# Kernel optimization log

Measured on AMD Instinct MI355X. Metric: run time of the kernel, lower is better.

Reference implementation:

```python
import math
import jax, jax.numpy as jnp
import numpy as np

HIDDEN = 1024
HEADS = 16
HEAD_DIM = HIDDEN // HEADS
PRIME = 7
MAX_ITERS = 10
ENT_THRESH = 0.2
PRIME_SCALE = 1.0 / math.sqrt(PRIME * HEAD_DIM)
EPS = 1e-6


def setup_inputs() -> dict:
    key = jax.random.key(0)
    ks = jax.random.split(key, 6)
    B, S = 2, 2048
    w = 0.02
    return {
        "hidden_states": jax.random.normal(ks[0], (B, S, HIDDEN), jnp.float32),
        "q_w": jax.random.normal(ks[1], (HIDDEN, HIDDEN), jnp.float32) * w,
        "q_b": jnp.zeros((HIDDEN,), jnp.float32),
        "k_w": jax.random.normal(ks[2], (HIDDEN, HIDDEN), jnp.float32) * w,
        "k_b": jnp.zeros((HIDDEN,), jnp.float32),
        "v_w": jax.random.normal(ks[3], (HIDDEN, HIDDEN), jnp.float32) * w,
        "v_b": jnp.zeros((HIDDEN,), jnp.float32),
        "o_w": jax.random.normal(ks[4], (HIDDEN, HIDDEN), jnp.float32) * w,
        "o_b": jnp.zeros((HIDDEN,), jnp.float32),
        "attention_mask": jnp.ones((B, S), jnp.int32),
    }


def _split_heads(x):
    B, S, _ = x.shape
    return x.reshape(B, S, HEADS, HEAD_DIM).transpose(0, 2, 1, 3)


def reference(hidden_states, q_w, q_b, k_w, k_b, v_w, v_b, o_w, o_b, attention_mask):
    B, S, _ = hidden_states.shape
    # projections (torch Linear: x @ W^T + b)
    q = _split_heads(hidden_states @ q_w.T + q_b) * PRIME_SCALE  # [B,H,S,hd]
    k = _split_heads(hidden_states @ k_w.T + k_b)
    v = _split_heads(hidden_states @ v_w.T + v_b)

    scores = jnp.einsum("bhqd,bhkd->bhqk", q, k)  # [B,H,S,S]
    mask = attention_mask[:, None, None, :]
    scores = jnp.where(mask == 0, -jnp.inf, scores)
    attn = jax.nn.softmax(scores, axis=-1)  # dropout p=0 (eval)

    base = jnp.einsum("bhqk,bhkd->bhqd", attn, v)  # attention_weights @ v

    # entropy of the (fixed) attention weights: [B,H]
    entropy = -jnp.sum(attn * jnp.log(attn + EPS), axis=-1).mean(axis=-1)
    avg_entropy = entropy.mean()

    # loop never changes attn, so entropy is constant: either break at i=1 or run all
    full = base
    for i in range(1, MAX_ITERS):
        blend = 1.0 / (1.0 + math.exp(-i / MAX_ITERS))          # sigmoid(i/max)
        res_scale = 0.5 + 0.5 * blend                            # resonance scale
        full = (1.0 - blend) * full + blend * (res_scale * base)

    out_heads = jnp.where(avg_entropy < ENT_THRESH, base, full)  # [B,H,S,hd]

    merged = out_heads.transpose(0, 2, 1, 3).reshape(B, S, HIDDEN)
    return merged @ o_w.T + o_b
```

## Files before the change

### kernel.cpp

```cpp
#include <hip/hip_runtime.h>
#include <hip/hip_bf16.h>
#include <stdint.h>


#define PRIME_SCALE 0.047245559126654356f
#define LOG2E       1.4426950408889634f
#define LN2         0.6931471805599453f
#define QSCALE      (PRIME_SCALE * LOG2E)
#define BLEND_C     0.85096556f

#if __has_builtin(__builtin_amdgcn_exp2f)
#define EXP2(x) __builtin_amdgcn_exp2f(x)
#else
#define EXP2(x) exp2f(x)
#endif

typedef __attribute__((ext_vector_type(8))) short short8;
typedef __attribute__((ext_vector_type(4))) float f32x4;

__device__ __forceinline__ unsigned short f2bf(float x) {
    union { float f; unsigned int u; } v; v.f = x;
    unsigned int r = (v.u + 0x7fffu + ((v.u >> 16) & 1u)) >> 16;
    return (unsigned short)r;
}
__device__ __forceinline__ unsigned short f2bf_fast(float x) {
    union { float f; unsigned int u; } v; v.f = x;
    return (unsigned short)((v.u + 0x8000u) >> 16);
}
__device__ __forceinline__ float bf2f(unsigned short x) {
    union { unsigned int u; float f; } v; v.u = ((unsigned int)x) << 16;
    return v.f;
}
__device__ __forceinline__ unsigned cvtpk_bf16(float lo, float hi) {
    unsigned r;
    asm("v_cvt_pk_bf16_f32 %0, %1, %2" : "=v"(r) : "v"(lo), "v"(hi));
    return r;
}

__device__ __forceinline__ void glds16(const unsigned short* g, unsigned short* l) {
    __builtin_amdgcn_global_load_lds((const __attribute__((address_space(1))) unsigned int*)g,
                                     (__attribute__((address_space(3))) unsigned int*)l,
                                     16, 0, 0);
}

__global__ void zero_out_f32(float* p, int n) {
    int i = blockIdx.x * 256 + threadIdx.x;
    if (i < n) p[i] = 0.f;
}

__global__ __launch_bounds__(256) void cvt5(
    const float* __restrict__ s0, const float* __restrict__ s1, const float* __restrict__ s2,
    const float* __restrict__ s3, const float* __restrict__ s4,
    unsigned short* __restrict__ d0, unsigned short* __restrict__ d1, unsigned short* __restrict__ d2,
    unsigned short* __restrict__ d3, unsigned short* __restrict__ d4, float* entp)
{
    if (blockIdx.x == 0 && threadIdx.x == 0) entp[0] = 0.f;
    unsigned int i = blockIdx.x * 256 + threadIdx.x;
    const float* s; unsigned short* d; unsigned int off;
    if (i < (1u << 20)) { s = s0; d = d0; off = i; }
    else {
        unsigned int j = i - (1u << 20);
        unsigned int sel = j >> 18; off = j & 0x3FFFFu;
        s = sel == 0 ? s1 : sel == 1 ? s2 : sel == 2 ? s3 : s4;
        d = sel == 0 ? d1 : sel == 1 ? d2 : sel == 2 ? d3 : d4;
    }
    float4 v = ((const float4*)s)[off];
    ushort4 p; p.x = f2bf(v.x); p.y = f2bf(v.y); p.z = f2bf(v.z); p.w = f2bf(v.w);
    ((ushort4*)d)[off] = p;
}

__global__ __launch_bounds__(256) void gemm_qkv(
    const unsigned short* __restrict__ hsb,
    const unsigned short* __restrict__ qwb, const unsigned short* __restrict__ kwb,
    const unsigned short* __restrict__ vwb,
    const float* __restrict__ qb, const float* __restrict__ kb, const float* __restrict__ vb,
    unsigned short* __restrict__ Qo, unsigned short* __restrict__ Ko, unsigned short* __restrict__ Vto)
{
    const int bid = blockIdx.x;
    const int x = bid & 7;
    const int i = bid >> 3;
    const int op = i >> 5;
    const int j = i & 31;
    const unsigned short *A, *B; const float* bias; unsigned short* C;
    int m0, n0, ldc, biasRow; float scale;
    if (op == 0)      { A = hsb; B = qwb; bias = qb; C = Qo;
                        m0 = (x * 4 + (j >> 3)) * 128; n0 = (j & 7) * 128;  ldc = 1024; biasRow = 0; scale = QSCALE; }
    else if (op == 1) { A = hsb; B = kwb; bias = kb; C = Ko;
                        m0 = (x * 4 + (j >> 3)) * 128; n0 = (j & 7) * 128;  ldc = 1024; biasRow = 0; scale = 1.f; }
    else              { A = vwb; B = hsb; bias = vb; C = Vto;
                        m0 = (j & 7) * 128; n0 = (x * 4 + (j >> 3)) * 128;  ldc = 4096; biasRow = 1; scale = 1.f; }

    __shared__ unsigned short As[128 * 32];
    __shared__ unsigned short Bs[128 * 32];
    const int t = threadIdx.x, lane = t & 63, w = t >> 6;
    const int quad = lane >> 4, l15 = lane & 15;
    const int wr = (w >> 1) * 64, wc = (w & 1) * 64;
    const int srow = lane >> 2, scol = (lane & 3) * 8;

    f32x4 acc[4][4];
#pragma unroll
    for (int ii = 0; ii < 4; ++ii)
#pragma unroll
        for (int jj = 0; jj < 4; ++jj) acc[ii][jj] = (f32x4){0.f, 0.f, 0.f, 0.f};

    for (int kk = 0; kk < 32; ++kk) {
        const int k0 = kk * 32;
#pragma unroll
        for (int jj = 0; jj < 2; ++jj) {
            int row = (w * 2 + jj) * 16 + srow;
            glds16(&A[(size_t)(m0 + row) * 1024 + k0 + scol], &As[(w * 2 + jj) * 512]);
            glds16(&B[(size_t)(n0 + row) * 1024 + k0 + scol], &Bs[(w * 2 + jj) * 512]);
        }
        __syncthreads();
        short8 af[4], bf[4];
#pragma unroll
        for (int mt = 0; mt < 4; ++mt) af[mt] = *(const short8*)&As[(wr + mt * 16 + l15) * 32 + quad * 8];
#pragma unroll
        for (int nt = 0; nt < 4; ++nt) bf[nt] = *(const short8*)&Bs[(wc + nt * 16 + l15) * 32 + quad * 8];
#pragma unroll
        for (int mt = 0; mt < 4; ++mt)
#pragma unroll
            for (int nt = 0; nt < 4; ++nt)
                acc[mt][nt] = __builtin_amdgcn_mfma_f32_16x16x32_bf16(af[mt], bf[nt], acc[mt][nt], 0, 0, 0);
        __syncthreads();
    }
#pragma unroll
    for (int mt = 0; mt < 4; ++mt) {
#pragma unroll
        for (int nt = 0; nt < 4; ++nt) {
            int n = n0 + wc + nt * 16 + l15;
#pragma unroll
            for (int r = 0; r < 4; ++r) {
                int m = m0 + wr + mt * 16 + quad * 4 + r;
                float bval = biasRow ? bias[m] : bias[n];
                C[(size_t)m * ldc + n] = f2bf((acc[mt][nt][r] + bval) * scale);
            }
        }
    }
}


#define STAGE(KT, BUF) do {                                                         \
    int kn_ = (KT) * 64;                                                            \
    _Pragma("unroll")                                                               \
    for (int i_ = 0; i_ < 2; ++i_) {                                                \
        int row_ = w * 16 + i_ * 8 + r8;                                            \
        int c_ = ch8 ^ (row_ & 7);                                                  \
        glds16(&K[(size_t)(b * 2048 + kn_ + row_) * 1024 + h * 64 + c_ * 8],        \
               &Ks[BUF][(w * 16 + i_ * 8) * 64]);                                   \
        glds16(&Vt[(size_t)(h * 64 + row_) * 4096 + b * 2048 + kn_ + c_ * 8],       \
               &Vs[BUF][(w * 16 + i_ * 8) * 64]);                                   \
    }                                                                               \
} while (0)

#define QK_SOFTMAX(MASKED)                                                          \
    _Pragma("unroll")                                                               \
    for (int nt = 0; nt < 4; ++nt) {                                                \
        int krow = nt * 16 + l15;                                                   \
        short8 kf0 = *(const short8*)&Ks[cur][krow * 64 + ((quad ^ (krow & 7)) * 8)];       \
        short8 kf1 = *(const short8*)&Ks[cur][krow * 64 + (((quad + 4) ^ (krow & 7)) * 8)]; \
        f32x4 sv[2];                                                                \
        __builtin_amdgcn_s_setprio(1);                                              \
        _Pragma("unroll")                                                           \
        for (int st = 0; st < 2; ++st) {                                            \
            sv[st] = __builtin_amdgcn_mfma_f32_16x16x32_bf16(kf0, qa[st][0], (f32x4){0.f, 0.f, 0.f, 0.f}, 0, 0, 0); \
            sv[st] = __builtin_amdgcn_mfma_f32_16x16x32_bf16(kf1, qa[st][1], sv[st], 0, 0, 0); \
        }                                                                           \
        __builtin_amdgcn_s_setprio(0);                                              \
        unsigned mb = 0xFu;                                                         \
        if (MASKED) {                                                               \
            unsigned mw = (nt & 2) ? mwB : mwA;                                     \
            mb = (mw >> (((nt & 1) << 4) + (quad << 2))) & 0xFu;                    \
        }                                                                           \
        _Pragma("unroll")                                                           \
        for (int st = 0; st < 2; ++st) {                                            \
            float s0 = sv[st][0], s1 = sv[st][1], s2 = sv[st][2], s3 = sv[st][3];   \
            if (MASKED) {                                                           \
                s0 = (mb & 1u) ? s0 : -1.0e30f;                                     \
                s1 = (mb & 2u) ? s1 : -1.0e30f;                                     \
                s2 = (mb & 4u) ? s2 : -1.0e30f;                                     \
                s3 = (mb & 8u) ? s3 : -1.0e30f;                                     \
            }                                                                       \
            float p0 = EXP2(s0), p1 = EXP2(s1), p2 = EXP2(s2), p3 = EXP2(s3);       \
            l_r[st] += (p0 + p1) + (p2 + p3);                                       \
            T_r[st] += (p0 * s0 + p1 * s1) + (p2 * s2 + p3 * s3);                   \
            pk[nt][st][0] = cvtpk_bf16(p0, p1);                                     \
            pk[nt][st][1] = cvtpk_bf16(p2, p3);                                     \
        }                                                                           \
    }

__global__ __launch_bounds__(256, 2) void flash_full(
    const unsigned short* __restrict__ Q,
    const unsigned short* __restrict__ K,
    const unsigned short* __restrict__ Vt,
    const int* __restrict__ mask,
    unsigned short* __restrict__ O,
    float* __restrict__ entp)
{
    const int ww = ((blockIdx.x & 7) << 6) + (blockIdx.x >> 3);
    const int qt = ww & 15;
    const int bh = ww >> 4;
    const int b = bh >> 4, h = bh & 15;
    const int t = threadIdx.x, lane = t & 63, w = t >> 6;
    const int quad = lane >> 4, l15 = lane & 15;
    const int r8 = lane >> 3, ch8 = lane & 7;

    __shared__ __align__(16) unsigned short Ks[2][64 * 64];
    __shared__ __align__(16) unsigned short Vs[2][64 * 64];
    __shared__ unsigned int maskBits[64];
    __shared__ float went[4];

    short8 qa[2][2];
#pragma unroll
    for (int st = 0; st < 2; ++st) {
        size_t qrow = (size_t)(b * 2048 + qt * 128 + w * 32 + st * 16 + l15) * 1024 + h * 64;
        union { uint4 v; short8 s8; } u0, u1;
        u0.v = *(const uint4*)&Q[qrow + quad * 8];
        u1.v = *(const uint4*)&Q[qrow + 32 + quad * 8];
        qa[st][0] = u0.s8; qa[st][1] = u1.s8;
    }

    {
        const int4* mp = (const int4*)(mask + b * 2048 + t * 8);
        int4 a = mp[0], c = mp[1];
        unsigned bits = (unsigned)(a.x != 0)       | ((unsigned)(a.y != 0) << 1)
                      | ((unsigned)(a.z != 0) << 2) | ((unsigned)(a.w != 0) << 3)
                      | ((unsigned)(c.x != 0) << 4) | ((unsigned)(c.y != 0) << 5)
                      | ((unsigned)(c.z != 0) << 6) | ((unsigned)(c.w != 0) << 7);
        ((unsigned char*)maskBits)[t] = (unsigned char)bits;
    }

    STAGE(0, 0);
    STAGE(1, 1);

    float l_r[2] = {0.f, 0.f}, T_r[2] = {0.f, 0.f};
    f32x4 o_acc[2][4];
#pragma unroll
    for (int st = 0; st < 2; ++st)
#pragma unroll
        for (int nt = 0; nt < 4; ++nt) o_acc[st][nt] = (f32x4){0.f, 0.f, 0.f, 0.f};

    asm volatile("s_waitcnt lgkmcnt(0)" ::: "memory");
    asm volatile("s_waitcnt vmcnt(4)" ::: "memory");
    asm volatile("s_barrier" ::: "memory");

    for (int kt = 0; kt < 32; ++kt) {
        const int cur = kt & 1;
        unsigned mwA = maskBits[kt * 2], mwB = maskBits[kt * 2 + 1];

        unsigned pk[4][2][2];
        if ((mwA & mwB) == 0xFFFFFFFFu) {
            QK_SOFTMAX(0)
        } else {
            QK_SOFTMAX(1)
        }

#pragma unroll
        for (int ks = 0; ks < 2; ++ks) {
            short8 pa[2];
#pragma unroll
            for (int st = 0; st < 2; ++st) {
                unsigned a0 = pk[2 * ks][st][0], a1 = pk[2 * ks][st][1];
                unsigned b0 = pk[2 * ks + 1][st][0], b1 = pk[2 * ks + 1][st][1];
                asm("v_permlane32_swap_b32 %0, %1" : "+v"(a0), "+v"(b0));
                asm("v_permlane32_swap_b32 %0, %1" : "+v"(a1), "+v"(b1));
                asm("v_permlane16_swap_b32 %0, %1" : "+v"(a0), "+v"(b0));
                asm("v_permlane16_swap_b32 %0, %1" : "+v"(a1), "+v"(b1));
                union { unsigned u[4]; short8 s8; } uu;
                uu.u[0] = a0; uu.u[1] = a1; uu.u[2] = b0; uu.u[3] = b1;
                pa[st] = uu.s8;
            }
            __builtin_amdgcn_s_setprio(1);
#pragma unroll
            for (int nt = 0; nt < 4; ++nt) {
                int vrow = nt * 16 + l15;
                short8 vf = *(const short8*)&Vs[cur][vrow * 64 + ((((ks * 4 + quad)) ^ (vrow & 7)) * 8)];
#pragma unroll
                for (int st = 0; st < 2; ++st)
                    o_acc[st][nt] = __builtin_amdgcn_mfma_f32_16x16x32_bf16(pa[st], vf, o_acc[st][nt], 0, 0, 0);
            }
            __builtin_amdgcn_s_setprio(0);
        }

        if (kt < 31) {
            asm volatile("s_barrier" ::: "memory");
            if (kt < 30) {
                STAGE(kt + 2, cur);
                asm volatile("s_waitcnt vmcnt(4)" ::: "memory");
            } else {
                asm volatile("s_waitcnt vmcnt(0)" ::: "memory");
            }
            asm volatile("s_barrier" ::: "memory");
        }
    }

    float ent_acc = 0.f;
#pragma unroll
    for (int st = 0; st < 2; ++st) {
        float l = l_r[st], T = T_r[st];
        l += __shfl_xor(l, 16); T += __shfl_xor(T, 16);
        l += __shfl_xor(l, 32); T += __shfl_xor(T, 32);
        ent_acc += __log2f(l) - T / l;
        float inv[4];
#pragma unroll
        for (int r = 0; r < 4; ++r)
            inv[r] = 1.0f / __shfl(l, quad * 4 + r);
#pragma unroll
        for (int r = 0; r < 4; ++r) {
            int mrow = b * 2048 + qt * 128 + w * 32 + st * 16 + quad * 4 + r;
#pragma unroll
            for (int nt = 0; nt < 4; ++nt)
                O[(size_t)mrow * 1024 + h * 64 + nt * 16 + l15] = f2bf_fast(o_acc[st][nt][r] * inv[r]);
        }
    }
    ent_acc += __shfl_xor(ent_acc, 1);
    ent_acc += __shfl_xor(ent_acc, 2);
    ent_acc += __shfl_xor(ent_acc, 4);
    ent_acc += __shfl_xor(ent_acc, 8);
    if (lane == 0) went[w] = ent_acc;
    __syncthreads();
    if (t == 0)
        atomicAdd(entp, LN2 * (went[0] + went[1] + went[2] + went[3]));
}

__global__ __launch_bounds__(256) void gemm_out_bf(
    const unsigned short* __restrict__ A, const unsigned short* __restrict__ Bw,
    const float* __restrict__ bias, const float* __restrict__ entp,
    float* __restrict__ C)
{
    const float avg = entp[0] * (1.0f / 65536.0f);
    const float scale = (avg < 0.2f) ? 1.0f : BLEND_C;

    const int x = blockIdx.x & 7;
    const int j = blockIdx.x >> 3;
    const int m0 = (x * 4 + (j >> 3)) * 128;
    const int n0 = (j & 7) * 128;
    __shared__ unsigned short As[128 * 32];
    __shared__ unsigned short Bs[128 * 32];
    const int t = threadIdx.x, lane = t & 63, w = t >> 6;
    const int quad = lane >> 4, l15 = lane & 15;
    const int wr = (w >> 1) * 64, wc = (w & 1) * 64;
    const int srow = lane >> 2, scol = (lane & 3) * 8;

    f32x4 acc[4][4];
#pragma unroll
    for (int ii = 0; ii < 4; ++ii)
#pragma unroll
        for (int jj = 0; jj < 4; ++jj) acc[ii][jj] = (f32x4){0.f, 0.f, 0.f, 0.f};

    for (int kk = 0; kk < 32; ++kk) {
        const int k0 = kk * 32;
#pragma unroll
        for (int jj = 0; jj < 2; ++jj) {
            int row = (w * 2 + jj) * 16 + srow;
            glds16(&A[(size_t)(m0 + row) * 1024 + k0 + scol], &As[(w * 2 + jj) * 512]);
            glds16(&Bw[(size_t)(n0 + row) * 1024 + k0 + scol], &Bs[(w * 2 + jj) * 512]);
        }
        __syncthreads();
        short8 af[4], bf[4];
#pragma unroll
        for (int mt = 0; mt < 4; ++mt) af[mt] = *(const short8*)&As[(wr + mt * 16 + l15) * 32 + quad * 8];
#pragma unroll
        for (int nt = 0; nt < 4; ++nt) bf[nt] = *(const short8*)&Bs[(wc + nt * 16 + l15) * 32 + quad * 8];
#pragma unroll
        for (int mt = 0; mt < 4; ++mt)
#pragma unroll
            for (int nt = 0; nt < 4; ++nt)
                acc[mt][nt] = __builtin_amdgcn_mfma_f32_16x16x32_bf16(af[mt], bf[nt], acc[mt][nt], 0, 0, 0);
        __syncthreads();
    }
#pragma unroll
    for (int mt = 0; mt < 4; ++mt) {
#pragma unroll
        for (int nt = 0; nt < 4; ++nt) {
            int n = n0 + wc + nt * 16 + l15;
#pragma unroll
            for (int r = 0; r < 4; ++r) {
                int m = m0 + wr + mt * 16 + quad * 4 + r;
                C[(size_t)m * 1024 + n] = scale * acc[mt][nt][r] + bias[n];
            }
        }
    }
}

extern "C" void kernel_launch(void* const* d_in, const int* in_sizes, int n_in,
                              void* d_out, int out_size, void* d_ws, size_t ws_size,
                              hipStream_t stream)
{
    const float* hs = (const float*)d_in[0];
    const float* qw = (const float*)d_in[1];
    const float* qb = (const float*)d_in[2];
    const float* kw = (const float*)d_in[3];
    const float* kb = (const float*)d_in[4];
    const float* vw = (const float*)d_in[5];
    const float* vb = (const float*)d_in[6];
    const float* ow = (const float*)d_in[7];
    const float* ob = (const float*)d_in[8];
    const int*   mask = (const int*)d_in[9];
    float* out = (float*)d_out;

    const size_t MB = 1024 * 1024;
    char* ws = (char*)d_ws;
    dim3 blk(256);

    if (ws_size >= 50 * MB) {
        unsigned short* hsb = (unsigned short*)(ws);
        unsigned short* Q   = (unsigned short*)(ws + 8 * MB);
        unsigned short* Kp  = (unsigned short*)(ws + 16 * MB);
        unsigned short* Vt  = (unsigned short*)(ws + 24 * MB);
        unsigned short* qwb = (unsigned short*)(ws + 32 * MB);
        unsigned short* kwb = (unsigned short*)(ws + 34 * MB);
        unsigned short* vwb = (unsigned short*)(ws + 36 * MB);
        unsigned short* owb = (unsigned short*)(ws + 38 * MB);
        float* entp         = (float*)(ws + 40 * MB);
        unsigned short* O   = hsb;

        cvt5<<<dim3(8192), blk, 0, stream>>>(hs, qw, kw, vw, ow, hsb, qwb, kwb, vwb, owb, entp);
        gemm_qkv<<<dim3(768), blk, 0, stream>>>(hsb, qwb, kwb, vwb, qb, kb, vb, Q, Kp, Vt);
        flash_full<<<dim3(512), blk, 0, stream>>>(Q, Kp, Vt, mask, O, entp);
        gemm_out_bf<<<dim3(256), blk, 0, stream>>>(O, owb, ob, entp, out);
    } else {
        zero_out_f32<<<dim3((out_size + 255) / 256), blk, 0, stream>>>(out, out_size);
    }
}
```

Before: 203.9 us.

## Fuse Q and K projections into one block sharing the hidden-state tile

The QKV projection kernel now computes the Q and K output tiles in the same block, loading the hidden-state A tile once and multiplying it against both the Q and K weight tiles into two accumulator sets. V blocks keep the single-accumulator path, and the grid drops from 768 to 512 blocks. This cuts redundant A-tile global loads and block count, but doubles accumulator registers for Q/K blocks, which risks occupancy even with the launch-bounds hint. It also creates load imbalance, since Q/K blocks do twice the work of V blocks.

```diff
diff --git a/kernel.cpp b/kernel.cpp
--- a/kernel.cpp
+++ b/kernel.cpp
@@ -69,39 +69,46 @@
     ((ushort4*)d)[off] = p;
 }
 
-__global__ __launch_bounds__(256) void gemm_qkv(
+__global__ __launch_bounds__(256, 2) void gemm_qkv(
     const unsigned short* __restrict__ hsb,
     const unsigned short* __restrict__ qwb, const unsigned short* __restrict__ kwb,
     const unsigned short* __restrict__ vwb,
     const float* __restrict__ qb, const float* __restrict__ kb, const float* __restrict__ vb,
     unsigned short* __restrict__ Qo, unsigned short* __restrict__ Ko, unsigned short* __restrict__ Vto)
 {
-    const int bid = blockIdx.x;
-    const int x = bid & 7;
-    const int i = bid >> 3;
-    const int op = i >> 5;
-    const int j = i & 31;
-    const unsigned short *A, *B; const float* bias; unsigned short* C;
-    int m0, n0, ldc, biasRow; float scale;
-    if (op == 0)      { A = hsb; B = qwb; bias = qb; C = Qo;
-                        m0 = (x * 4 + (j >> 3)) * 128; n0 = (j & 7) * 128;  ldc = 1024; biasRow = 0; scale = QSCALE; }
-    else if (op == 1) { A = hsb; B = kwb; bias = kb; C = Ko;
-                        m0 = (x * 4 + (j >> 3)) * 128; n0 = (j & 7) * 128;  ldc = 1024; biasRow = 0; scale = 1.f; }
-    else              { A = vwb; B = hsb; bias = vb; C = Vto;
-                        m0 = (j & 7) * 128; n0 = (x * 4 + (j >> 3)) * 128;  ldc = 4096; biasRow = 1; scale = 1.f; }
+    const int x = blockIdx.x & 7;
+    const int i = blockIdx.x >> 3;
+    const bool isQK = (i < 32);
+    const int j = isQK ? i : i - 32;
 
     __shared__ unsigned short As[128 * 32];
-    __shared__ unsigned short Bs[128 * 32];
+    __shared__ unsigned short B0s[128 * 32];
+    __shared__ unsigned short B1s[128 * 32];
     const int t = threadIdx.x, lane = t & 63, w = t >> 6;
     const int quad = lane >> 4, l15 = lane & 15;
     const int wr = (w >> 1) * 64, wc = (w & 1) * 64;
     const int srow = lane >> 2, scol = (lane & 3) * 8;
 
-    f32x4 acc[4][4];
+    const unsigned short *A, *B0;
+    int m0, n0;
+    if (isQK) {
+        m0 = (x * 4 + (j >> 3)) * 128;
+        n0 = (j & 7) * 128;
+        A = hsb; B0 = qwb;
+    } else {
+        m0 = (j & 7) * 128;
+        n0 = (x * 4 + (j >> 3)) * 128;
+        A = vwb; B0 = hsb;
+    }
+
+    f32x4 acc0[4][4], acc1[4][4];
 #pragma unroll
     for (int ii = 0; ii < 4; ++ii)
 #pragma unroll
-        for (int jj = 0; jj < 4; ++jj) acc[ii][jj] = (f32x4){0.f, 0.f, 0.f, 0.f};
+        for (int jj = 0; jj < 4; ++jj) {
+            acc0[ii][jj] = (f32x4){0.f, 0.f, 0.f, 0.f};
+            acc1[ii][jj] = (f32x4){0.f, 0.f, 0.f, 0.f};
+        }
 
     for (int kk = 0; kk < 32; ++kk) {
         const int k0 = kk * 32;
@@ -109,31 +116,59 @@
         for (int jj = 0; jj < 2; ++jj) {
             int row = (w * 2 + jj) * 16 + srow;
             glds16(&A[(size_t)(m0 + row) * 1024 + k0 + scol], &As[(w * 2 + jj) * 512]);
-            glds16(&B[(size_t)(n0 + row) * 1024 + k0 + scol], &Bs[(w * 2 + jj) * 512]);
+            glds16(&B0[(size_t)(n0 + row) * 1024 + k0 + scol], &B0s[(w * 2 + jj) * 512]);
+            if (isQK)
+                glds16(&kwb[(size_t)(n0 + row) * 1024 + k0 + scol], &B1s[(w * 2 + jj) * 512]);
         }
         __syncthreads();
-        short8 af[4], bf[4];
+        short8 af[4], bf0[4];
 #pragma unroll
         for (int mt = 0; mt < 4; ++mt) af[mt] = *(const short8*)&As[(wr + mt * 16 + l15) * 32 + quad * 8];
 #pragma unroll
-        for (int nt = 0; nt < 4; ++nt) bf[nt] = *(const short8*)&Bs[(wc + nt * 16 + l15) * 32 + quad * 8];
+        for (int nt = 0; nt < 4; ++nt) bf0[nt] = *(const short8*)&B0s[(wc + nt * 16 + l15) * 32 + quad * 8];
 #pragma unroll
         for (int mt = 0; mt < 4; ++mt)
 #pragma unroll
             for (int nt = 0; nt < 4; ++nt)
-                acc[mt][nt] = __builtin_amdgcn_mfma_f32_16x16x32_bf16(af[mt], bf[nt], acc[mt][nt], 0, 0, 0);
+                acc0[mt][nt] = __builtin_amdgcn_mfma_f32_16x16x32_bf16(af[mt], bf0[nt], acc0[mt][nt], 0, 0, 0);
+        if (isQK) {
+            short8 bf1[4];
+#pragma unroll
+            for (int nt = 0; nt < 4; ++nt) bf1[nt] = *(const short8*)&B1s[(wc + nt * 16 + l15) * 32 + quad * 8];
+#pragma unroll
+            for (int mt = 0; mt < 4; ++mt)
+#pragma unroll
+                for (int nt = 0; nt < 4; ++nt)
+                    acc1[mt][nt] = __builtin_amdgcn_mfma_f32_16x16x32_bf16(af[mt], bf1[nt], acc1[mt][nt], 0, 0, 0);
+        }
         __syncthreads();
     }
-#pragma unroll
-    for (int mt = 0; mt < 4; ++mt) {
-#pragma unroll
-        for (int nt = 0; nt < 4; ++nt) {
-            int n = n0 + wc + nt * 16 + l15;
-#pragma unroll
-            for (int r = 0; r < 4; ++r) {
-                int m = m0 + wr + mt * 16 + quad * 4 + r;
-                float bval = biasRow ? bias[m] : bias[n];
-                C[(size_t)m * ldc + n] = f2bf((acc[mt][nt][r] + bval) * scale);
+
+    if (isQK) {
+#pragma unroll
+        for (int mt = 0; mt < 4; ++mt) {
+#pragma unroll
+            for (int nt = 0; nt < 4; ++nt) {
+                int n = n0 + wc + nt * 16 + l15;
+#pragma unroll
+                for (int r = 0; r < 4; ++r) {
+                    int m = m0 + wr + mt * 16 + quad * 4 + r;
+                    Qo[(size_t)m * 1024 + n] = f2bf((acc0[mt][nt][r] + qb[n]) * QSCALE);
+                    Ko[(size_t)m * 1024 + n] = f2bf(acc1[mt][nt][r] + kb[n]);
+                }
+            }
+        }
+    } else {
+#pragma unroll
+        for (int mt = 0; mt < 4; ++mt) {
+#pragma unroll
+            for (int nt = 0; nt < 4; ++nt) {
+                int n = n0 + wc + nt * 16 + l15;
+#pragma unroll
+                for (int r = 0; r < 4; ++r) {
+                    int m = m0 + wr + mt * 16 + quad * 4 + r;
+                    Vto[(size_t)m * 4096 + n] = f2bf(acc0[mt][nt][r] + vb[m]);
+                }
             }
         }
     }
@@ -416,7 +451,7 @@
         unsigned short* O   = hsb;
 
         cvt5<<<dim3(8192), blk, 0, stream>>>(hs, qw, kw, vw, ow, hsb, qwb, kwb, vwb, owb, entp);
-        gemm_qkv<<<dim3(768), blk, 0, stream>>>(hsb, qwb, kwb, vwb, qb, kb, vb, Q, Kp, Vt);
+        gemm_qkv<<<dim3(512), blk, 0, stream>>>(hsb, qwb, kwb, vwb, qb, kb, vb, Q, Kp, Vt);
         flash_full<<<dim3(512), blk, 0, stream>>>(Q, Kp, Vt, mask, O, entp);
         gemm_out_bf<<<dim3(256), blk, 0, stream>>>(O, owb, ob, entp, out);
     } else {
```

Result: slower. 210.0 us (+3.0%).
